# Kernel tuning notes

Hardware: AMD Instinct MI355X
Metric: run time of the kernel (lower is better)

The kernel has to match this reference:

```python
import jax, jax.numpy as jnp
import numpy as np

B, S, HID = 2, 2048, 2048
NH, NKV, D = 16, 8, 128
EPS = 1e-6
THETA = 10000.0


def _rms_norm(x, w):
    # RMSNorm over last dim (head_dim), Qwen3-style per-head q/k norm
    var = jnp.mean(jnp.square(x), axis=-1, keepdims=True)
    return x * jax.lax.rsqrt(var + EPS) * w


def _rotate_half(x):
    x1, x2 = jnp.split(x, 2, axis=-1)
    return jnp.concatenate([-x2, x1], axis=-1)


def setup_inputs() -> dict:
    key = jax.random.key(0)
    ks = jax.random.split(key, 8)
    hidden_states = jax.random.normal(ks[0], (B, S, HID), dtype=jnp.float32)
    # rotary embeddings (HF-style: emb = concat(freqs, freqs))
    inv_freq = 1.0 / (THETA ** (jnp.arange(0, D, 2, dtype=jnp.float32) / D))
    pos = jnp.arange(S, dtype=jnp.float32)
    freqs = jnp.outer(pos, inv_freq)                      # [S, D/2]
    emb = jnp.concatenate([freqs, freqs], axis=-1)        # [S, D]
    cos = jnp.broadcast_to(jnp.cos(emb)[None], (B, S, D))
    sin = jnp.broadcast_to(jnp.sin(emb)[None], (B, S, D))
    w_scale = 1.0 / np.sqrt(HID)
    Wq = jax.random.normal(ks[1], (HID, NH * D), dtype=jnp.float32) * w_scale
    Wk = jax.random.normal(ks[2], (HID, NKV * D), dtype=jnp.float32) * w_scale
    Wv = jax.random.normal(ks[3], (HID, NKV * D), dtype=jnp.float32) * w_scale
    Wo = jax.random.normal(ks[4], (NH * D, HID), dtype=jnp.float32) * w_scale
    q_norm_w = jnp.ones((D,), dtype=jnp.float32)
    k_norm_w = jnp.ones((D,), dtype=jnp.float32)
    return {"hidden_states": hidden_states, "cos": cos, "sin": sin,
            "Wq": Wq, "Wk": Wk, "Wv": Wv, "Wo": Wo,
            "q_norm_w": q_norm_w, "k_norm_w": k_norm_w}


def reference(hidden_states, cos, sin, Wq, Wk, Wv, Wo, q_norm_w, k_norm_w):
    b, s, _ = hidden_states.shape
    # projections + per-head RMSNorm on q/k, then [B,H,S,D]
    q = _rms_norm((hidden_states @ Wq).reshape(b, s, NH, D), q_norm_w)
    k = _rms_norm((hidden_states @ Wk).reshape(b, s, NKV, D), k_norm_w)
    v = (hidden_states @ Wv).reshape(b, s, NKV, D)
    q = jnp.swapaxes(q, 1, 2)  # [B,NH,S,D]
    k = jnp.swapaxes(k, 1, 2)  # [B,NKV,S,D]
    v = jnp.swapaxes(v, 1, 2)
    # rotary position embedding
    c = cos[:, None, :, :]
    sn = sin[:, None, :, :]
    q = q * c + _rotate_half(q) * sn
    k = k * c + _rotate_half(k) * sn
    # GQA: expand kv heads to match query heads
    rep = NH // NKV
    k = jnp.repeat(k, rep, axis=1)
    v = jnp.repeat(v, rep, axis=1)
    # scaled causal attention (splash_attention semantics, causal mask)
    q = q * (D ** -0.5)
    scores = jnp.einsum('bhqd,bhkd->bhqk', q, k)
    causal = jnp.tril(jnp.ones((s, s), dtype=bool))
    scores = jnp.where(causal[None, None], scores, jnp.finfo(scores.dtype).min)
    attn = jax.nn.softmax(scores, axis=-1)
    out = jnp.einsum('bhqk,bhkd->bhqd', attn, v)
    out = jnp.swapaxes(out, 1, 2).reshape(b, s, NH * D)
    return out @ Wo
```

## Files before the change

kernel.cpp:

```cpp
#include <hip/hip_runtime.h>
#include <hip/hip_bf16.h>

typedef unsigned short u16;
typedef unsigned int u32;
typedef unsigned long long u64;
typedef __attribute__((ext_vector_type(8))) short short8;
typedef __attribute__((ext_vector_type(4))) float floatx4;

#define AS1 __attribute__((address_space(1)))
#define AS3 __attribute__((address_space(3)))

__device__ __forceinline__ float bf2f(u16 u) {
    u32 x = ((u32)u) << 16;
    float f;
    __builtin_memcpy(&f, &x, 4);
    return f;
}
__device__ __forceinline__ u16 f2bf(float f) {
    u32 x;
    __builtin_memcpy(&x, &f, 4);
    u32 r = (x + 0x7fffu + ((x >> 16) & 1u)) >> 16;
    return (u16)r;
}
__device__ __forceinline__ u32 f2bf_pk(float a, float b) {
    __hip_bfloat162 h = __float22bfloat162_rn(float2{a, b});
    u32 r;
    __builtin_memcpy(&r, &h, 4);
    return r;
}

__global__ __launch_bounds__(1024) void prep_weights(const float* __restrict__ Wq,
                                                     const float* __restrict__ Wk,
                                                     const float* __restrict__ Wv,
                                                     const float* __restrict__ Wo,
                                                     const float* __restrict__ X,
                                                     u16* __restrict__ WqkvT,
                                                     u16* __restrict__ WoT,
                                                     u16* __restrict__ Xb) {
    const int z = blockIdx.z;
    const int tx = threadIdx.x, ty = threadIdx.y;
    if (z == 4) {
        int idx = blockIdx.y * 64 + blockIdx.x;
        if (idx >= 2048) return;
        int tid = ty * 32 + tx;
        size_t i = (size_t)idx * 4096 + (size_t)tid * 4;
        float4 v = *(const float4*)(X + i);
        u16 o[4] = {f2bf(v.x), f2bf(v.y), f2bf(v.z), f2bf(v.w)};
        *(u64*)(Xb + i) = *(u64*)o;
        return;
    }
    const float* in;
    u16* out;
    int C;
    if (z == 0) { in = Wq; out = WqkvT; C = 2048; }
    else if (z == 1) { in = Wk; out = WqkvT + 2048 * 2048; C = 1024; }
    else if (z == 2) { in = Wv; out = WqkvT + 3072 * 2048; C = 1024; }
    else { in = Wo; out = WoT; C = 2048; }
    const int c0 = blockIdx.x * 32, r0 = blockIdx.y * 32;
    if (c0 >= C) return;
    __shared__ u16 t[32][33];
    t[ty][tx] = f2bf(in[(size_t)(r0 + ty) * C + c0 + tx]);
    __syncthreads();
    out[(size_t)(c0 + ty) * 2048 + r0 + tx] = t[tx][ty];
}

template <typename OUT_T>
__global__ __launch_bounds__(512, 2) void gemm256(const u16* __restrict__ A,
                                                  const u16* __restrict__ Bt,
                                                  OUT_T* __restrict__ C,
                                                  int M, int N, int K) {
    (void)M;
    __shared__ __align__(16) u16 lds[2][2][2][128 * 64];
    const int tid = threadIdx.x;
    const int wave = tid >> 6, lane = tid & 63;
    const int lr = lane & 15, lq = lane >> 4;
    const int wm = wave >> 2, wn = wave & 3;
    const int m0 = blockIdx.y * 256, n0 = blockIdx.x * 256;

    const int srow = lane >> 3;
    const int schunk = ((lane & 7) ^ srow) << 3;
    const int slot = wave << 1;

    auto stage = [&](const u16* src, int rbase, int buf, int mat, int half, int k0) {
#pragma unroll
        for (int j = 0; j < 2; j++) {
            int r = rbase + half * 128 + (slot + j) * 8 + srow;
            __builtin_amdgcn_global_load_lds(
                (const AS1 void*)(src + (size_t)r * K + k0 + schunk),
                (AS3 void*)(&lds[buf][mat][half][(slot + j) * 512]), 16, 0, 0);
        }
    };

    floatx4 zf = {0.f, 0.f, 0.f, 0.f};
    floatx4 acc[8][4];
#pragma unroll
    for (int i = 0; i < 8; i++)
#pragma unroll
        for (int jn = 0; jn < 4; jn++) acc[i][jn] = zf;

    const int NT = K >> 6;

    stage(Bt, n0, 0, 1, 0, 0);
    stage(Bt, n0, 0, 1, 1, 0);
    stage(A, m0, 0, 0, 0, 0);
    stage(A, m0, 0, 0, 1, 0);
    if (NT > 1) {
        stage(Bt, n0, 1, 1, 0, 64);
        stage(Bt, n0, 1, 1, 1, 64);
        stage(A, m0, 1, 0, 0, 64);
        asm volatile("s_waitcnt vmcnt(6)" ::: "memory");
    } else {
        asm volatile("s_waitcnt vmcnt(0)" ::: "memory");
    }
    __builtin_amdgcn_s_barrier();

    for (int kt = 0; kt < NT; kt++) {
        const int b = kt & 1;
        const u16* Ab = &lds[b][0][wm][0];
        const u16* Bb = &lds[b][1][wn >> 1][0];
        const int brow = (wn & 1) * 64;
        const int sx = lr & 7;
        const int nk = (kt + 2) << 6;

        short8 bf0[4], bf1[4], af[4];
#pragma unroll
        for (int jn = 0; jn < 4; jn++) {
            int rh = brow + jn * 16 + lr;
            bf0[jn] = *(const short8*)(Bb + rh * 64 + ((lq ^ sx) << 3));
            bf1[jn] = *(const short8*)(Bb + rh * 64 + (((4 + lq) ^ sx) << 3));
        }
#pragma unroll
        for (int i = 0; i < 4; i++)
            af[i] = *(const short8*)(Ab + (i * 16 + lr) * 64 + ((lq ^ sx) << 3));
        if (kt + 1 < NT) stage(A, m0, b ^ 1, 0, 1, (kt + 1) << 6);
        __builtin_amdgcn_s_barrier();
        asm volatile("s_waitcnt lgkmcnt(0)" ::: "memory");
        __builtin_amdgcn_sched_barrier(0);
        __builtin_amdgcn_s_setprio(1);
#pragma unroll
        for (int i = 0; i < 4; i++)
#pragma unroll
            for (int jn = 0; jn < 4; jn++)
                acc[i][jn] = __builtin_amdgcn_mfma_f32_16x16x32_bf16(af[i], bf0[jn], acc[i][jn], 0, 0, 0);
        __builtin_amdgcn_s_setprio(0);
        __builtin_amdgcn_s_barrier();

        short8 ag[4];
#pragma unroll
        for (int i = 0; i < 4; i++)
            ag[i] = *(const short8*)(Ab + ((i + 4) * 16 + lr) * 64 + ((lq ^ sx) << 3));
        if (kt + 2 < NT) stage(Bt, n0, b, 1, 0, nk);
        __builtin_amdgcn_s_barrier();
        asm volatile("s_waitcnt lgkmcnt(0)" ::: "memory");
        __builtin_amdgcn_sched_barrier(0);
        __builtin_amdgcn_s_setprio(1);
#pragma unroll
        for (int i = 0; i < 4; i++)
#pragma unroll
            for (int jn = 0; jn < 4; jn++)
                acc[i + 4][jn] = __builtin_amdgcn_mfma_f32_16x16x32_bf16(ag[i], bf0[jn], acc[i + 4][jn], 0, 0, 0);
        __builtin_amdgcn_s_setprio(0);
        __builtin_amdgcn_s_barrier();

        short8 c0[4], c1[4];
#pragma unroll
        for (int i = 0; i < 4; i++) {
            c0[i] = *(const short8*)(Ab + (i * 16 + lr) * 64 + (((4 + lq) ^ sx) << 3));
            c1[i] = *(const short8*)(Ab + ((i + 4) * 16 + lr) * 64 + (((4 + lq) ^ sx) << 3));
        }
        if (kt + 2 < NT) stage(Bt, n0, b, 1, 1, nk);
        __builtin_amdgcn_s_barrier();
        asm volatile("s_waitcnt lgkmcnt(0)" ::: "memory");
        __builtin_amdgcn_sched_barrier(0);
        __builtin_amdgcn_s_setprio(1);
#pragma unroll
        for (int i = 0; i < 4; i++)
#pragma unroll
            for (int jn = 0; jn < 4; jn++)
                acc[i][jn] = __builtin_amdgcn_mfma_f32_16x16x32_bf16(c0[i], bf1[jn], acc[i][jn], 0, 0, 0);
        __builtin_amdgcn_s_setprio(0);
        __builtin_amdgcn_s_barrier();

        if (kt + 2 < NT) stage(A, m0, b, 0, 0, nk);
        __builtin_amdgcn_s_barrier();
        __builtin_amdgcn_s_setprio(1);
#pragma unroll
        for (int i = 0; i < 4; i++)
#pragma unroll
            for (int jn = 0; jn < 4; jn++)
                acc[i + 4][jn] = __builtin_amdgcn_mfma_f32_16x16x32_bf16(c1[i], bf1[jn], acc[i + 4][jn], 0, 0, 0);
        __builtin_amdgcn_s_setprio(0);
        if (kt + 2 < NT) asm volatile("s_waitcnt vmcnt(6)" ::: "memory");
        else asm volatile("s_waitcnt vmcnt(0)" ::: "memory");
        __builtin_amdgcn_s_barrier();
    }

#pragma unroll
    for (int i = 0; i < 8; i++)
#pragma unroll
        for (int jn = 0; jn < 4; jn++)
#pragma unroll
            for (int r = 0; r < 4; r++) {
                int row = m0 + wm * 128 + i * 16 + lq * 4 + r;
                int col = n0 + wn * 64 + jn * 16 + lr;
                if constexpr (sizeof(OUT_T) == 2)
                    C[(size_t)row * N + col] = f2bf(acc[i][jn][r]);
                else
                    C[(size_t)row * N + col] = acc[i][jn][r];
            }
}

template <typename OUT_T>
__global__ __launch_bounds__(512, 2) void gemm128n(const u16* __restrict__ A,
                                                   const u16* __restrict__ Bt,
                                                   OUT_T* __restrict__ C,
                                                   int M, int N, int K) {
    (void)M;
    __shared__ __align__(16) u16 Abuf[2][2][128 * 64];
    __shared__ __align__(16) u16 Bbuf[2][128 * 64];
    const int tid = threadIdx.x;
    const int wave = tid >> 6, lane = tid & 63;
    const int lr = lane & 15, lq = lane >> 4;
    const int wm = wave >> 1, wn = wave & 1;
    const int m0 = blockIdx.y * 256, n0 = blockIdx.x * 128;

    const int srow = lane >> 3;
    const int schunk = ((lane & 7) ^ srow) << 3;
    const int slot = wave << 1;

    auto stage = [&](const u16* src, int rowbase, u16* ldsbase, int k0) {
#pragma unroll
        for (int j = 0; j < 2; j++) {
            int r = rowbase + (slot + j) * 8 + srow;
            __builtin_amdgcn_global_load_lds(
                (const AS1 void*)(src + (size_t)r * K + k0 + schunk),
                (AS3 void*)(ldsbase + (slot + j) * 512), 16, 0, 0);
        }
    };

    floatx4 zf = {0.f, 0.f, 0.f, 0.f};
    floatx4 acc[4][4];
#pragma unroll
    for (int i = 0; i < 4; i++)
#pragma unroll
        for (int jn = 0; jn < 4; jn++) acc[i][jn] = zf;

    const int NT = K >> 6;

    stage(A, m0, &Abuf[0][0][0], 0);
    stage(A, m0 + 128, &Abuf[0][1][0], 0);
    stage(Bt, n0, &Bbuf[0][0], 0);
    if (NT > 1) {
        stage(A, m0, &Abuf[1][0][0], 64);
        stage(Bt, n0, &Bbuf[1][0], 64);
        asm volatile("s_waitcnt vmcnt(4)" ::: "memory");
    } else {
        asm volatile("s_waitcnt vmcnt(0)" ::: "memory");
    }
    __builtin_amdgcn_s_barrier();

    for (int kt = 0; kt < NT; kt++) {
        const int b = kt & 1;
        const u16* Ab = &Abuf[b][wm >> 1][0];
        const u16* Bb = &Bbuf[b][0];
        const int ar = (wm & 1) * 64;
        const int br = wn * 64;
        const int sx = lr & 7;
        const int nk = (kt + 2) << 6;

        short8 bf0[4], bf1[4], af[4];
#pragma unroll
        for (int jn = 0; jn < 4; jn++) {
            int rh = br + jn * 16 + lr;
            bf0[jn] = *(const short8*)(Bb + rh * 64 + ((lq ^ sx) << 3));
            bf1[jn] = *(const short8*)(Bb + rh * 64 + (((4 + lq) ^ sx) << 3));
        }
#pragma unroll
        for (int i = 0; i < 4; i++)
            af[i] = *(const short8*)(Ab + (ar + i * 16 + lr) * 64 + ((lq ^ sx) << 3));
        if (kt + 1 < NT) stage(A, m0 + 128, &Abuf[b ^ 1][1][0], (kt + 1) << 6);
        __builtin_amdgcn_s_barrier();
        asm volatile("s_waitcnt lgkmcnt(0)" ::: "memory");
        __builtin_amdgcn_sched_barrier(0);
        __builtin_amdgcn_s_setprio(1);
#pragma unroll
        for (int i = 0; i < 2; i++)
#pragma unroll
            for (int jn = 0; jn < 4; jn++)
                acc[i][jn] = __builtin_amdgcn_mfma_f32_16x16x32_bf16(af[i], bf0[jn], acc[i][jn], 0, 0, 0);
        __builtin_amdgcn_s_setprio(0);
        __builtin_amdgcn_s_barrier();

        if (kt + 2 < NT) stage(Bt, n0, &Bbuf[b][0], nk);
        __builtin_amdgcn_s_barrier();
        __builtin_amdgcn_s_setprio(1);
#pragma unroll
        for (int i = 2; i < 4; i++)
#pragma unroll
            for (int jn = 0; jn < 4; jn++)
                acc[i][jn] = __builtin_amdgcn_mfma_f32_16x16x32_bf16(af[i], bf0[jn], acc[i][jn], 0, 0, 0);
        __builtin_amdgcn_s_setprio(0);
        __builtin_amdgcn_s_barrier();

        short8 ag[4];
#pragma unroll
        for (int i = 0; i < 4; i++)
            ag[i] = *(const short8*)(Ab + (ar + i * 16 + lr) * 64 + (((4 + lq) ^ sx) << 3));
        __builtin_amdgcn_s_barrier();
        asm volatile("s_waitcnt lgkmcnt(0)" ::: "memory");
        __builtin_amdgcn_sched_barrier(0);
        __builtin_amdgcn_s_setprio(1);
#pragma unroll
        for (int i = 0; i < 2; i++)
#pragma unroll
            for (int jn = 0; jn < 4; jn++)
                acc[i][jn] = __builtin_amdgcn_mfma_f32_16x16x32_bf16(ag[i], bf1[jn], acc[i][jn], 0, 0, 0);
        __builtin_amdgcn_s_setprio(0);
        __builtin_amdgcn_s_barrier();

        if (kt + 2 < NT) stage(A, m0, &Abuf[b][0][0], nk);
        __builtin_amdgcn_s_barrier();
        __builtin_amdgcn_s_setprio(1);
#pragma unroll
        for (int i = 2; i < 4; i++)
#pragma unroll
            for (int jn = 0; jn < 4; jn++)
                acc[i][jn] = __builtin_amdgcn_mfma_f32_16x16x32_bf16(ag[i], bf1[jn], acc[i][jn], 0, 0, 0);
        __builtin_amdgcn_s_setprio(0);
        if (kt + 2 < NT) asm volatile("s_waitcnt vmcnt(4)" ::: "memory");
        else asm volatile("s_waitcnt vmcnt(0)" ::: "memory");
        __builtin_amdgcn_s_barrier();
    }

#pragma unroll
    for (int i = 0; i < 4; i++)
#pragma unroll
        for (int jn = 0; jn < 4; jn++)
#pragma unroll
            for (int r = 0; r < 4; r++) {
                int row = m0 + wm * 64 + i * 16 + lq * 4 + r;
                int col = n0 + wn * 64 + jn * 16 + lr;
                if constexpr (sizeof(OUT_T) == 2)
                    C[(size_t)row * N + col] = f2bf(acc[i][jn][r]);
                else
                    C[(size_t)row * N + col] = acc[i][jn][r];
            }
}

__global__ __launch_bounds__(256) void prep_qkv(u16* __restrict__ QKV,
                                                u16* __restrict__ Vt,
                                                const float* __restrict__ cosb,
                                                const float* __restrict__ sinb,
                                                const float* __restrict__ qw,
                                                const float* __restrict__ kw) {
    const int bx = blockIdx.x;
    const int tid = threadIdx.x;
    if (bx >= 24576) {
        const int idx = bx - 24576;
        const int s0 = (idx & 63) * 32;
        const int d0 = ((idx >> 6) & 3) * 32;
        const int zz = idx >> 8;
        const int b = zz >> 3, kv = zz & 7;
        __shared__ u16 t[32][33];
        const int tx = tid & 31, ty0 = tid >> 5;
#pragma unroll
        for (int p = 0; p < 4; p++) {
            int r = ty0 + p * 8;
            t[r][tx] = QKV[(size_t)(b * 2048 + s0 + r) * 4096 + 3072 + kv * 128 + d0 + tx];
        }
        __syncthreads();
#pragma unroll
        for (int p = 0; p < 4; p++) {
            int r = ty0 + p * 8;
            Vt[(size_t)((b * 8 + kv) * 128 + d0 + r) * 2048 + s0 + tx] = t[tx][r];
        }
        return;
    }
    const int wave = tid >> 6, lane = tid & 63;
    const int t = bx * 4 + wave;
    u16* ptr;
    const float* w;
    float scale;
    int bs;
    if (t < 65536) {
        bs = t >> 4;
        ptr = QKV + (size_t)bs * 4096 + (t & 15) * 128;
        w = qw;
        scale = 0.08838834764831845f * 1.4426950408889634f;
    } else {
        int t2 = t - 65536;
        bs = t2 >> 3;
        ptr = QKV + (size_t)bs * 4096 + 2048 + (t2 & 7) * 128;
        w = kw;
        scale = 1.0f;
    }
    const int d = lane * 2;
    u32 xv = *(const u32*)(ptr + d);
    float x0 = bf2f((u16)(xv & 0xffff)), x1 = bf2f((u16)(xv >> 16));
    float ss = x0 * x0 + x1 * x1;
#pragma unroll
    for (int off = 1; off < 64; off <<= 1) ss += __shfl_xor(ss, off);
    float rn = rsqrtf(ss * (1.0f / 128.0f) + 1e-6f);
    float2 wv = *(const float2*)(w + d);
    float y0 = x0 * rn * wv.x;
    float y1 = x1 * rn * wv.y;
    float p0 = __shfl_xor(y0, 32);
    float p1 = __shfl_xor(y1, 32);
    float sgn = (lane < 32) ? -1.0f : 1.0f;
    float2 cv = *(const float2*)(cosb + (size_t)bs * 128 + d);
    float2 sv = *(const float2*)(sinb + (size_t)bs * 128 + d);
    float o0 = (y0 * cv.x + sgn * p0 * sv.x) * scale;
    float o1 = (y1 * cv.y + sgn * p1 * sv.y) * scale;
    *(u32*)(ptr + d) = (u32)f2bf(o0) | ((u32)f2bf(o1) << 16);
}

__global__ __launch_bounds__(256, 3) void attn_kernel(const u16* __restrict__ QKV,
                                                      const u16* __restrict__ Vt,
                                                      u16* __restrict__ O) {
    __shared__ __align__(16) u16 Ks[2][64 * 128];
    __shared__ __align__(16) u16 Vs[144 * 64];
    const int tid = threadIdx.x;
    const int wave = tid >> 6, lane = tid & 63;
    const int lr = lane & 15, lq = lane >> 4;

    const int id = blockIdx.x;
    const int qt = 31 - (id >> 5);
    const int j = id & 31;
    const int h = j & 15;
    const int b = j >> 4;

    const int kv = h >> 1;
    const int q0 = qt * 64;
    const int wq = wave * 16;

    auto stageK = [&](int buf, int k0s) {
#pragma unroll
        for (int jj = 0; jj < 4; jj++) {
            int r = wave * 16 + jj * 4 + (lane >> 4);
            int ch = (lane & 15) ^ (r & 15);
            __builtin_amdgcn_global_load_lds(
                (const AS1 void*)(QKV + (size_t)(b * 2048 + k0s + r) * 4096 + 2048 + kv * 128 + ch * 8),
                (AS3 void*)(&Ks[buf][(wave * 16 + jj * 4) * 128]), 16, 0, 0);
        }
    };
    auto stageV = [&](int k0s) {
#pragma unroll
        for (int jj = 0; jj < 4; jj++) {
            int r = wave * 32 + jj * 8 + (lane >> 3);
            int ch = (lane & 7) ^ (r & 7);
            __builtin_amdgcn_global_load_lds(
                (const AS1 void*)(Vt + (size_t)((b * 8 + kv) * 128 + r) * 2048 + k0s + ch * 8),
                (AS3 void*)(&Vs[(wave * 32 + jj * 8) * 64]), 16, 0, 0);
        }
    };

    *(u64*)(&Vs[128 * 64 + tid * 4]) = 0x3F803F803F803F80ULL;
    asm volatile("s_waitcnt lgkmcnt(0)" ::: "memory");

    short8 qf[4];
#pragma unroll
    for (int t = 0; t < 4; t++)
        qf[t] = *(const short8*)(QKV + (size_t)(b * 2048 + q0 + wq + lr) * 4096 + h * 128 + t * 32 + lq * 8);

    floatx4 zf = {0.f, 0.f, 0.f, 0.f};
    floatx4 oacc[9];
#pragma unroll
    for (int jn = 0; jn < 9; jn++) oacc[jn] = zf;
    float mstate = -1e30f;

    const int nIter = qt + 1;

    stageK(0, 0);

    for (int kt = 0; kt < nIter; kt++) {
        const int k0 = kt * 64;
        const int cur = kt & 1;
        asm volatile("s_waitcnt vmcnt(0)" ::: "memory");
        __builtin_amdgcn_s_barrier();
        stageV(k0);
        if (kt + 1 < nIter) stageK(cur ^ 1, k0 + 64);

        const bool active = (k0 <= q0 + wq + 15);
        u64 pb[4];
        if (active) {
            const u16* KsC = &Ks[cur][0];
            floatx4 sacc[4];
#pragma unroll
            for (int jm = 0; jm < 4; jm++) sacc[jm] = zf;
            __builtin_amdgcn_s_setprio(1);
#pragma unroll
            for (int t = 0; t < 4; t++) {
                short8 a[4];
#pragma unroll
                for (int jm = 0; jm < 4; jm++)
                    a[jm] = *(const short8*)(KsC + (jm * 16 + lr) * 128 + (((t * 4 + lq) ^ lr) << 3));
#pragma unroll
                for (int jm = 0; jm < 4; jm++)
                    sacc[jm] = __builtin_amdgcn_mfma_f32_16x16x32_bf16(a[jm], qf[t], sacc[jm], 0, 0, 0);
            }
            __builtin_amdgcn_s_setprio(0);

            if (k0 + 63 > q0 + wq) {
#pragma unroll
                for (int jm = 0; jm < 4; jm++) {
                    int diff = (q0 + wq + lr) - (k0 + jm * 16 + lq * 4);
#pragma unroll
                    for (int r = 0; r < 4; r++)
                        if (r > diff) sacc[jm][r] = -1e30f;
                }
            }

            float mx = -1e30f;
#pragma unroll
            for (int jm = 0; jm < 4; jm++) {
                float a0 = fmaxf(sacc[jm][0], sacc[jm][1]);
                float a1 = fmaxf(sacc[jm][2], sacc[jm][3]);
                mx = fmaxf(mx, fmaxf(a0, a1));
            }
            mx = fmaxf(mx, __shfl_xor(mx, 16));
            mx = fmaxf(mx, __shfl_xor(mx, 32));

            bool defer = __all(mx - mstate <= 8.0f);
            float mnew = defer ? mstate : fmaxf(mstate, mx);

#pragma unroll
            for (int jm = 0; jm < 4; jm++)
#pragma unroll
                for (int r = 0; r < 4; r++)
                    sacc[jm][r] = exp2f(sacc[jm][r] - mnew);

            if (!defer) {
                float alpha = exp2f(mstate - mnew);
                mstate = mnew;
                float ao[4];
#pragma unroll
                for (int r = 0; r < 4; r++) ao[r] = __shfl(alpha, lq * 4 + r);
#pragma unroll
                for (int jn = 0; jn < 9; jn++)
#pragma unroll
                    for (int r = 0; r < 4; r++) oacc[jn][r] *= ao[r];
            }

#pragma unroll
            for (int jm = 0; jm < 4; jm++) {
                u32 lo = f2bf_pk(sacc[jm][0], sacc[jm][1]);
                u32 hi = f2bf_pk(sacc[jm][2], sacc[jm][3]);
                pb[jm] = (u64)lo | ((u64)hi << 32);
            }
        }

        if (kt + 1 < nIter) asm volatile("s_waitcnt vmcnt(4)" ::: "memory");
        else                asm volatile("s_waitcnt vmcnt(0)" ::: "memory");
        __builtin_amdgcn_s_barrier();

        if (active) {
            __builtin_amdgcn_s_setprio(1);
#pragma unroll
            for (int t = 0; t < 2; t++) {
                union { short8 v; u64 q[2]; } pa;
                pa.q[0] = pb[2 * t];
                pa.q[1] = pb[2 * t + 1];
#pragma unroll
                for (int jn = 0; jn < 9; jn++) {
                    const u16* vrow = Vs + (jn * 16 + lr) * 64 + (lq & 1) * 4;
                    union { short8 v; u64 q[2]; } vb;
                    vb.q[0] = *(const u64*)(vrow + (((t * 4 + (lq >> 1)) ^ (lr & 7)) << 3));
                    vb.q[1] = *(const u64*)(vrow + (((t * 4 + 2 + (lq >> 1)) ^ (lr & 7)) << 3));
                    oacc[jn] = __builtin_amdgcn_mfma_f32_16x16x32_bf16(pa.v, vb.v, oacc[jn], 0, 0, 0);
                }
            }
            __builtin_amdgcn_s_setprio(0);
        }
    }

#pragma unroll
    for (int jn = 0; jn < 8; jn++)
#pragma unroll
        for (int r = 0; r < 4; r++) {
            int row = q0 + wq + lq * 4 + r;
            O[(size_t)(b * 2048 + row) * 2048 + h * 128 + jn * 16 + lr] =
                f2bf(oacc[jn][r] / oacc[8][r]);
        }
}

extern "C" void kernel_launch(void* const* d_in, const int* in_sizes, int n_in,
                              void* d_out, int out_size, void* d_ws, size_t ws_size,
                              hipStream_t stream) {
    const float* X = (const float*)d_in[0];
    const float* cosb = (const float*)d_in[1];
    const float* sinb = (const float*)d_in[2];
    const float* Wq = (const float*)d_in[3];
    const float* Wk = (const float*)d_in[4];
    const float* Wv = (const float*)d_in[5];
    const float* Wo = (const float*)d_in[6];
    const float* qw = (const float*)d_in[7];
    const float* kw = (const float*)d_in[8];
    float* out = (float*)d_out;
    u16* ws = (u16*)d_ws;

    u16* WqkvT = ws;
    u16* WoT = WqkvT + 8388608;
    u16* Xb = WoT + 4194304;
    u16* QKVb = Xb + 8388608;
    u16* Vtb = QKVb + 16777216;
    u16* Ob = Xb;

    prep_weights<<<dim3(64, 64, 5), dim3(32, 32), 0, stream>>>(Wq, Wk, Wv, Wo, X,
                                                               WqkvT, WoT, Xb);

    gemm256<u16><<<dim3(16, 16), 512, 0, stream>>>(Xb, WqkvT, QKVb, 4096, 4096, 2048);

    prep_qkv<<<28672, 256, 0, stream>>>(QKVb, Vtb, cosb, sinb, qw, kw);

    attn_kernel<<<1024, 256, 0, stream>>>(QKVb, Vtb, Ob);

    gemm128n<float><<<dim3(16, 16), 512, 0, stream>>>(Ob, WoT, out, 4096, 2048, 2048);
}
```

Before: 363.2 us.

## Widen memory accesses in weight prep, V transpose, and QK norm/rope kernels

Moves the weight-conversion transposes to 64x64 tiles with 256-thread blocks, each thread moving packed pairs of bf16 values, and has the X conversion loop over 8 float4 chunks per thread. The V transpose in prep_qkv also uses 64x64 tiles with 32-bit packed loads and stores. The q/k RMSNorm+RoPE path now handles two heads per wave, four elements per lane, with 64-bit loads and stores. The aim is fewer, wider memory transactions and less launch and block overhead in these bandwidth-bound prep kernels, at the cost of more complex indexing and fewer blocks.

```diff
diff --git a/kernel.cpp b/kernel.cpp
--- a/kernel.cpp
+++ b/kernel.cpp
@@ -29,24 +29,28 @@
     return r;
 }
 
-__global__ __launch_bounds__(1024) void prep_weights(const float* __restrict__ Wq,
-                                                     const float* __restrict__ Wk,
-                                                     const float* __restrict__ Wv,
-                                                     const float* __restrict__ Wo,
-                                                     const float* __restrict__ X,
-                                                     u16* __restrict__ WqkvT,
-                                                     u16* __restrict__ WoT,
-                                                     u16* __restrict__ Xb) {
+__global__ __launch_bounds__(256) void prep_weights(const float* __restrict__ Wq,
+                                                    const float* __restrict__ Wk,
+                                                    const float* __restrict__ Wv,
+                                                    const float* __restrict__ Wo,
+                                                    const float* __restrict__ X,
+                                                    u16* __restrict__ WqkvT,
+                                                    u16* __restrict__ WoT,
+                                                    u16* __restrict__ Xb) {
     const int z = blockIdx.z;
     const int tx = threadIdx.x, ty = threadIdx.y;
     if (z == 4) {
-        int idx = blockIdx.y * 64 + blockIdx.x;
-        if (idx >= 2048) return;
         int tid = ty * 32 + tx;
-        size_t i = (size_t)idx * 4096 + (size_t)tid * 4;
-        float4 v = *(const float4*)(X + i);
-        u16 o[4] = {f2bf(v.x), f2bf(v.y), f2bf(v.z), f2bf(v.w)};
-        *(u64*)(Xb + i) = *(u64*)o;
+        int idx = blockIdx.y * 32 + blockIdx.x;
+        if (idx >= 1024) return;
+        size_t base = (size_t)idx * 256 + tid;
+#pragma unroll
+        for (int p = 0; p < 8; p++) {
+            size_t i = (base + (size_t)p * 262144) * 4;
+            float4 v = *(const float4*)(X + i);
+            u16 o[4] = {f2bf(v.x), f2bf(v.y), f2bf(v.z), f2bf(v.w)};
+            *(u64*)(Xb + i) = *(u64*)o;
+        }
         return;
     }
     const float* in;
@@ -56,12 +60,29 @@
     else if (z == 1) { in = Wk; out = WqkvT + 2048 * 2048; C = 1024; }
     else if (z == 2) { in = Wv; out = WqkvT + 3072 * 2048; C = 1024; }
     else { in = Wo; out = WoT; C = 2048; }
-    const int c0 = blockIdx.x * 32, r0 = blockIdx.y * 32;
+    const int c0 = blockIdx.x * 64, r0 = blockIdx.y * 64;
     if (c0 >= C) return;
-    __shared__ u16 t[32][33];
-    t[ty][tx] = f2bf(in[(size_t)(r0 + ty) * C + c0 + tx]);
+    __shared__ u16 t[64][66];
+#pragma unroll
+    for (int p = 0; p < 4; p++) {
+        int rr = (ty + 8 * p) * 2;
+#pragma unroll
+        for (int i = 0; i < 2; i++) {
+            float2 v = *(const float2*)(in + (size_t)(r0 + rr + i) * C + c0 + tx * 2);
+            *(u32*)&t[rr + i][tx * 2] = f2bf_pk(v.x, v.y);
+        }
+    }
     __syncthreads();
-    out[(size_t)(c0 + ty) * 2048 + r0 + tx] = t[tx][ty];
+#pragma unroll
+    for (int p = 0; p < 4; p++) {
+        int cc = (ty + 8 * p) * 2;
+        u32 a = *(const u32*)&t[tx * 2][cc];
+        u32 bq = *(const u32*)&t[tx * 2 + 1][cc];
+        u32 pk0 = (a & 0xffffu) | (bq << 16);
+        u32 pk1 = (a >> 16) | (bq & 0xffff0000u);
+        *(u32*)(out + (size_t)(c0 + cc) * 2048 + r0 + tx * 2) = pk0;
+        *(u32*)(out + (size_t)(c0 + cc + 1) * 2048 + r0 + tx * 2) = pk1;
+    }
 }
 
 template <typename OUT_T>
@@ -355,63 +376,78 @@
                                                 const float* __restrict__ kw) {
     const int bx = blockIdx.x;
     const int tid = threadIdx.x;
-    if (bx >= 24576) {
-        const int idx = bx - 24576;
-        const int s0 = (idx & 63) * 32;
-        const int d0 = ((idx >> 6) & 3) * 32;
-        const int zz = idx >> 8;
+    if (bx >= 12288) {
+        const int idx = bx - 12288;
+        const int s0 = (idx & 31) * 64;
+        const int d0 = ((idx >> 5) & 1) * 64;
+        const int zz = idx >> 6;
         const int b = zz >> 3, kv = zz & 7;
-        __shared__ u16 t[32][33];
-        const int tx = tid & 31, ty0 = tid >> 5;
+        __shared__ u16 t[64][66];
+        const int tx = tid & 31, ty = tid >> 5;
+        const u16* src = QKV + (size_t)(b * 2048 + s0) * 4096 + 3072 + kv * 128 + d0;
 #pragma unroll
         for (int p = 0; p < 4; p++) {
-            int r = ty0 + p * 8;
-            t[r][tx] = QKV[(size_t)(b * 2048 + s0 + r) * 4096 + 3072 + kv * 128 + d0 + tx];
+            int rr = (ty + 8 * p) * 2;
+#pragma unroll
+            for (int i = 0; i < 2; i++)
+                *(u32*)&t[rr + i][tx * 2] = *(const u32*)(src + (size_t)(rr + i) * 4096 + tx * 2);
         }
         __syncthreads();
+        u16* dst = Vt + (size_t)((b * 8 + kv) * 128 + d0) * 2048 + s0;
 #pragma unroll
         for (int p = 0; p < 4; p++) {
-            int r = ty0 + p * 8;
-            Vt[(size_t)((b * 8 + kv) * 128 + d0 + r) * 2048 + s0 + tx] = t[tx][r];
+            int cc = (ty + 8 * p) * 2;
+            u32 a = *(const u32*)&t[tx * 2][cc];
+            u32 bq = *(const u32*)&t[tx * 2 + 1][cc];
+            u32 pk0 = (a & 0xffffu) | (bq << 16);
+            u32 pk1 = (a >> 16) | (bq & 0xffff0000u);
+            *(u32*)(dst + (size_t)cc * 2048 + tx * 2) = pk0;
+            *(u32*)(dst + (size_t)(cc + 1) * 2048 + tx * 2) = pk1;
         }
         return;
     }
     const int wave = tid >> 6, lane = tid & 63;
+    const int half = lane >> 5, l5 = lane & 31;
     const int t = bx * 4 + wave;
+    const int R = t * 2 + half;
     u16* ptr;
     const float* w;
     float scale;
     int bs;
-    if (t < 65536) {
-        bs = t >> 4;
-        ptr = QKV + (size_t)bs * 4096 + (t & 15) * 128;
+    if (R < 65536) {
+        bs = R >> 4;
+        ptr = QKV + (size_t)bs * 4096 + (R & 15) * 128;
         w = qw;
         scale = 0.08838834764831845f * 1.4426950408889634f;
     } else {
-        int t2 = t - 65536;
-        bs = t2 >> 3;
-        ptr = QKV + (size_t)bs * 4096 + 2048 + (t2 & 7) * 128;
+        int R2 = R - 65536;
+        bs = R2 >> 3;
+        ptr = QKV + (size_t)bs * 4096 + 2048 + (R2 & 7) * 128;
         w = kw;
         scale = 1.0f;
     }
-    const int d = lane * 2;
-    u32 xv = *(const u32*)(ptr + d);
-    float x0 = bf2f((u16)(xv & 0xffff)), x1 = bf2f((u16)(xv >> 16));
-    float ss = x0 * x0 + x1 * x1;
-#pragma unroll
-    for (int off = 1; off < 64; off <<= 1) ss += __shfl_xor(ss, off);
+    const int d = l5 * 4;
+    u64 xv = *(const u64*)(ptr + d);
+    float x0 = bf2f((u16)xv), x1 = bf2f((u16)(xv >> 16));
+    float x2 = bf2f((u16)(xv >> 32)), x3 = bf2f((u16)(xv >> 48));
+    float ss = x0 * x0 + x1 * x1 + x2 * x2 + x3 * x3;
+#pragma unroll
+    for (int off = 1; off < 32; off <<= 1) ss += __shfl_xor(ss, off);
     float rn = rsqrtf(ss * (1.0f / 128.0f) + 1e-6f);
-    float2 wv = *(const float2*)(w + d);
-    float y0 = x0 * rn * wv.x;
-    float y1 = x1 * rn * wv.y;
-    float p0 = __shfl_xor(y0, 32);
-    float p1 = __shfl_xor(y1, 32);
-    float sgn = (lane < 32) ? -1.0f : 1.0f;
-    float2 cv = *(const float2*)(cosb + (size_t)bs * 128 + d);
-    float2 sv = *(const float2*)(sinb + (size_t)bs * 128 + d);
+    float4 wv = *(const float4*)(w + d);
+    float y0 = x0 * rn * wv.x, y1 = x1 * rn * wv.y;
+    float y2 = x2 * rn * wv.z, y3 = x3 * rn * wv.w;
+    float p0 = __shfl_xor(y0, 16), p1 = __shfl_xor(y1, 16);
+    float p2 = __shfl_xor(y2, 16), p3 = __shfl_xor(y3, 16);
+    float sgn = (l5 < 16) ? -1.0f : 1.0f;
+    float4 cv = *(const float4*)(cosb + (size_t)bs * 128 + d);
+    float4 sv = *(const float4*)(sinb + (size_t)bs * 128 + d);
     float o0 = (y0 * cv.x + sgn * p0 * sv.x) * scale;
     float o1 = (y1 * cv.y + sgn * p1 * sv.y) * scale;
-    *(u32*)(ptr + d) = (u32)f2bf(o0) | ((u32)f2bf(o1) << 16);
+    float o2 = (y2 * cv.z + sgn * p2 * sv.z) * scale;
+    float o3 = (y3 * cv.w + sgn * p3 * sv.w) * scale;
+    u64 res = (u64)f2bf_pk(o0, o1) | ((u64)f2bf_pk(o2, o3) << 32);
+    *(u64*)(ptr + d) = res;
 }
 
 __global__ __launch_bounds__(256, 3) void attn_kernel(const u16* __restrict__ QKV,
@@ -605,12 +641,12 @@
     u16* Vtb = QKVb + 16777216;
     u16* Ob = Xb;
 
-    prep_weights<<<dim3(64, 64, 5), dim3(32, 32), 0, stream>>>(Wq, Wk, Wv, Wo, X,
-                                                               WqkvT, WoT, Xb);
+    prep_weights<<<dim3(32, 32, 5), dim3(32, 8), 0, stream>>>(Wq, Wk, Wv, Wo, X,
+                                                              WqkvT, WoT, Xb);
 
     gemm256<u16><<<dim3(16, 16), 512, 0, stream>>>(Xb, WqkvT, QKVb, 4096, 4096, 2048);
 
-    prep_qkv<<<28672, 256, 0, stream>>>(QKVb, Vtb, cosb, sinb, qw, kw);
+    prep_qkv<<<13312, 256, 0, stream>>>(QKVb, Vtb, cosb, sinb, qw, kw);
 
     attn_kernel<<<1024, 256, 0, stream>>>(QKVb, Vtb, Ob);
 
```

Result: faster. 342.6 us (-5.7%).
